# Performance work log

Hardware: AMD Instinct MI355X
Metric: run time of the kernel (lower is better)

The kernel has to match this reference:

```python
import jax, jax.numpy as jnp
import numpy as np

NUM_PARTS = 2
SAMPLE_STEP = 3  # models sample_points(pts, 3, True) as deterministic stride-3 subsampling


def quat_to_rot(q):
    # wxyz quaternion -> 3x3 rotation (same formula as the torch module)
    q = q / jnp.linalg.norm(q)
    a, b, c, d = q[0], q[1], q[2], q[3]
    return jnp.stack([
        1 - 2 * c * c - 2 * d * d, 2 * b * c - 2 * a * d, 2 * a * c + 2 * b * d,
        2 * b * c + 2 * a * d, 1 - 2 * b * b - 2 * d * d, 2 * c * d - 2 * a * b,
        2 * b * d - 2 * a * c, 2 * a * b + 2 * c * d, 1 - 2 * b * b - 2 * c * c,
    ]).reshape(3, 3)


def make_transform(q, t):
    rot = quat_to_rot(q)                      # (3,3)
    top = jnp.concatenate([rot, t], axis=1)   # (3,4)
    bottom = jnp.array([[0.0, 0.0, 0.0, 1.0]], dtype=top.dtype)
    return jnp.concatenate([top, bottom], axis=0)  # (4,4)


def chamfer(x, y):
    # x: (M,4), y: (M,4) homogeneous points; symmetric chamfer of Euclidean cdist
    d2 = jnp.sum(x * x, -1)[:, None] + jnp.sum(y * y, -1)[None, :] - 2.0 * (x @ y.T)
    d = jnp.sqrt(jnp.maximum(d2, 0.0))
    return jnp.mean(jnp.min(d, axis=1)) + jnp.mean(jnp.min(d, axis=0))


def setup_inputs() -> dict:
    key = jax.random.key(0)
    ks = jax.random.split(key, 6)
    N = 24576
    camera_pts = jax.random.normal(ks[0], (NUM_PARTS, N, 3), dtype=jnp.float32)
    cad_pts = jax.random.normal(ks[1], (NUM_PARTS, N, 3), dtype=jnp.float32)
    part_weight = jax.random.uniform(ks[2], (NUM_PARTS + 1,), dtype=jnp.float32)
    rot_quat = jax.random.normal(ks[3], (NUM_PARTS, 4), dtype=jnp.float32)
    tra = jax.random.normal(ks[4], (NUM_PARTS, 3, 1), dtype=jnp.float32)
    joint_axes = jax.random.normal(ks[5], (NUM_PARTS, 2, 4), dtype=jnp.float32)
    return {"camera_pts": camera_pts, "cad_pts": cad_pts, "part_weight": part_weight,
            "rot_quat": rot_quat, "tra": tra, "joint_axes": joint_axes}


def reference(camera_pts, cad_pts, part_weight, rot_quat, tra, joint_axes):
    # stride-3 subsample, then homogenize with a ones column
    scad = cad_pts[:, ::SAMPLE_STEP]      # (P, M, 3)
    scam = camera_pts[:, ::SAMPLE_STEP]   # (P, M, 3)
    ones = jnp.ones(scad.shape[:-1] + (1,), dtype=scad.dtype)
    scad_h = jnp.concatenate([scad, ones], axis=-1)  # (P, M, 4)
    scam_h = jnp.concatenate([scam, ones], axis=-1)  # (P, M, 4)

    transforms = jax.vmap(make_transform)(rot_quat, tra)        # (P, 4, 4)
    cad_base = jnp.einsum('pij,pnj->pni', transforms, scad_h)   # (P, M, 4)

    e_geo_parts = jax.vmap(chamfer)(cad_base, scam_h)           # (P,)
    e_geo = jnp.dot(part_weight[:NUM_PARTS], e_geo_parts)

    diff = transforms[0] @ joint_axes[0].T - transforms[1] @ joint_axes[1].T  # (4, K)
    e_kin = jax.nn.sigmoid(-5.0 * jnp.linalg.norm(diff))

    all_objective = e_geo + part_weight[NUM_PARTS] * e_kin
    return all_objective, e_kin, jax.lax.stop_gradient(transforms)
```

## Files before the change

kernel.cpp:

```cpp
#include <hip/hip_runtime.h>
#include <math.h>

#define NS 8192
#define NPTS 24576

#define BXC 64
#define XPT 16
#define XB (NS / (BXC * XPT))
#define YSPLIT 64
#define YTILE (NS / YSPLIT)

#define RB 256
#define RBLOCKS (4 * (NS / RB))

typedef __attribute__((ext_vector_type(2))) float f32x2;


__device__ inline void build_transform(const float* __restrict__ rot_quat,
                                       const float* __restrict__ tra,
                                       int p, float* t) {
    float a = rot_quat[p * 4 + 0], b = rot_quat[p * 4 + 1];
    float c = rot_quat[p * 4 + 2], d = rot_quat[p * 4 + 3];
    float inv = rsqrtf(a * a + b * b + c * c + d * d);
    a *= inv; b *= inv; c *= inv; d *= inv;
    t[0]  = 1.f - 2.f * c * c - 2.f * d * d;
    t[1]  = 2.f * b * c - 2.f * a * d;
    t[2]  = 2.f * a * c + 2.f * b * d;
    t[3]  = tra[p * 3 + 0];
    t[4]  = 2.f * b * c + 2.f * a * d;
    t[5]  = 1.f - 2.f * b * b - 2.f * d * d;
    t[6]  = 2.f * c * d - 2.f * a * b;
    t[7]  = tra[p * 3 + 1];
    t[8]  = 2.f * b * d - 2.f * a * c;
    t[9]  = 2.f * a * b + 2.f * c * d;
    t[10] = 1.f - 2.f * b * b - 2.f * c * c;
    t[11] = tra[p * 3 + 2];
    t[12] = 0.f; t[13] = 0.f; t[14] = 0.f; t[15] = 1.f;
}

__global__ void pack_kernel(const float* __restrict__ cam_pts,
                            const float* __restrict__ cad_pts,
                            const float* __restrict__ rot_quat,
                            const float* __restrict__ tra,
                            const float* __restrict__ joint_axes,
                            float* __restrict__ ws,
                            float4* __restrict__ pts,
                            float* __restrict__ out) {
    int gid = blockIdx.x * blockDim.x + threadIdx.x;
    int p = gid >> 13;
    int i = gid & (NS - 1);

    float T[16];
    build_transform(rot_quat, tra, p, T);

    int base = p * NPTS * 3 + i * 9;
    float x = cad_pts[base], y = cad_pts[base + 1], z = cad_pts[base + 2];
    float q0 = fmaf(T[0], x, fmaf(T[1], y, fmaf(T[2],  z, T[3])));
    float q1 = fmaf(T[4], x, fmaf(T[5], y, fmaf(T[6],  z, T[7])));
    float q2 = fmaf(T[8], x, fmaf(T[9], y, fmaf(T[10], z, T[11])));
    pts[p * NS + i] = make_float4(q0, q1, q2, fmaf(q0, q0, fmaf(q1, q1, q2 * q2)));
    float cx = cam_pts[base], cy = cam_pts[base + 1], cz = cam_pts[base + 2];
    pts[2 * NS + p * NS + i] =
        make_float4(cx, cy, cz, fmaf(cx, cx, fmaf(cy, cy, cz * cz)));

    if (gid == 0) {
        float T0[16], T1[16];
        build_transform(rot_quat, tra, 0, T0);
        build_transform(rot_quat, tra, 1, T1);
        for (int k = 0; k < 16; ++k) { out[2 + k] = T0[k]; out[18 + k] = T1[k]; }
        float ss = 0.f;
        for (int r = 0; r < 4; ++r)
            for (int j = 0; j < 2; ++j) {
                float d0 = 0.f, d1 = 0.f;
                for (int k = 0; k < 4; ++k) {
                    d0 += T0[r * 4 + k] * joint_axes[j * 4 + k];
                    d1 += T1[r * 4 + k] * joint_axes[8 + j * 4 + k];
                }
                float df = d0 - d1;
                ss += df * df;
            }
        float ek = 1.f / (1.f + expf(5.f * sqrtf(ss)));
        ws[36] = ek;
        out[1] = ek;
        ws[0] = 0.f; ws[1] = 0.f; ws[2] = 0.f; ws[3] = 0.f;
        ((unsigned*)ws)[37] = 0u;
    }
}

__global__ __launch_bounds__(BXC) void chamfer_kernel(const float4* __restrict__ pts,
                                                      float* __restrict__ partial) {
    int combo = blockIdx.y;
    int p   = combo >> 1;
    int dir = combo & 1;
    const float4* X = pts + (dir == 0 ? p * NS : 2 * NS + p * NS);
    const float4* Y = pts + (dir == 0 ? 2 * NS + p * NS : p * NS);
    int ys = blockIdx.z;
    int xb = blockIdx.x;
    int t  = threadIdx.x;

    __shared__ float4 sy[YTILE];

    int xbase = xb * (BXC * XPT) + t;
    f32x2 m0[XPT / 2], m1[XPT / 2], m2[XPT / 2], s[XPT / 2], dmin[XPT / 2];
#pragma unroll
    for (int g = 0; g < XPT / 2; ++g) {
        float4 v0 = X[xbase + (2 * g) * BXC];
        float4 v1 = X[xbase + (2 * g + 1) * BXC];
        m0[g] = (f32x2){-2.f * v0.x, -2.f * v1.x};
        m1[g] = (f32x2){-2.f * v0.y, -2.f * v1.y};
        m2[g] = (f32x2){-2.f * v0.z, -2.f * v1.z};
        s[g]  = (f32x2){v0.w, v1.w};
        dmin[g] = (f32x2){3.4e38f, 3.4e38f};
    }

    int ybase = ys * YTILE;
#pragma unroll
    for (int c = 0; c < YTILE / BXC; ++c)
        sy[t + c * BXC] = Y[ybase + c * BXC + t];
    __syncthreads();

#pragma unroll 4
    for (int j = 0; j < YTILE; ++j) {
        float4 y = sy[j];
        f32x2 yw = (f32x2){y.w, y.w};
        f32x2 yx = (f32x2){y.x, y.x};
        f32x2 yy = (f32x2){y.y, y.y};
        f32x2 yz = (f32x2){y.z, y.z};
#pragma unroll
        for (int g = 0; g < XPT / 2; ++g) {
            f32x2 d = __builtin_elementwise_fma(m0[g], yx, yw);
            d = __builtin_elementwise_fma(m1[g], yy, d);
            d = __builtin_elementwise_fma(m2[g], yz, d);
            dmin[g] = __builtin_elementwise_min(dmin[g], d);
        }
    }

    float* prow = partial + (combo * YSPLIT + ys) * NS + xbase;
#pragma unroll
    for (int g = 0; g < XPT / 2; ++g) {
        f32x2 v = dmin[g] + s[g];
        prow[(2 * g) * BXC]     = v.x;
        prow[(2 * g + 1) * BXC] = v.y;
    }
}

__global__ void reduce_kernel(const float* __restrict__ partial,
                              const float* __restrict__ pw,
                              float* __restrict__ ws,
                              float* __restrict__ out) {
    int combo = blockIdx.y;
    int x = blockIdx.x * RB + threadIdx.x;
    const float* p = partial + combo * (YSPLIT * NS) + x;
    float m = 3.4e38f;
#pragma unroll 8
    for (int ysi = 0; ysi < YSPLIT; ++ysi) m = fminf(m, p[ysi * NS]);
    float d = sqrtf(fmaxf(m, 0.f));
#pragma unroll
    for (int off = 32; off > 0; off >>= 1) d += __shfl_down(d, off, 64);
    __shared__ float sm[RB / 64];
    int wid = threadIdx.x >> 6;
    if ((threadIdx.x & 63) == 0) sm[wid] = d;
    __syncthreads();
    if (threadIdx.x == 0) {
        float sum = 0.f;
        for (int w = 0; w < RB / 64; ++w) sum += sm[w];
        atomicAdd(&ws[combo], sum);
        __threadfence();
        unsigned old = atomicAdd(&((unsigned*)ws)[37], 1u);
        if (old == RBLOCKS - 1) {
            float a0 = atomicAdd(&ws[0], 0.f);
            float a1 = atomicAdd(&ws[1], 0.f);
            float a2 = atomicAdd(&ws[2], 0.f);
            float a3 = atomicAdd(&ws[3], 0.f);
            float e0 = (a0 + a1) * (1.f / NS);
            float e1 = (a2 + a3) * (1.f / NS);
            out[0] = pw[0] * e0 + pw[1] * e1 + pw[2] * ws[36];
        }
    }
}

extern "C" void kernel_launch(void* const* d_in, const int* in_sizes, int n_in,
                              void* d_out, int out_size, void* d_ws, size_t ws_size,
                              hipStream_t stream) {
    const float* cam = (const float*)d_in[0];
    const float* cad = (const float*)d_in[1];
    const float* pw  = (const float*)d_in[2];
    const float* rq  = (const float*)d_in[3];
    const float* tr  = (const float*)d_in[4];
    const float* ja  = (const float*)d_in[5];
    float* out = (float*)d_out;
    float* ws  = (float*)d_ws;
    float4* pts = (float4*)(ws + 64);
    float* partial = ws + 64 + 16 * NS;

    pack_kernel<<<(2 * NS) / 256, 256, 0, stream>>>(cam, cad, rq, tr, ja, ws, pts, out);
    dim3 cg(XB, 4, YSPLIT);
    chamfer_kernel<<<cg, BXC, 0, stream>>>(pts, partial);
    reduce_kernel<<<dim3(NS / RB, 4), RB, 0, stream>>>(partial, pw, ws, out);
}
```

Measured before the change: 105.2 us.

## Fuse point packing and transform into chamfer kernel, drop pack launch

Removes the separate pack kernel. Each chamfer block now loads the raw strided points itself, applies the rigid transform and computes squared norms on the fly. The transform output, the kinematic term and the workspace zeroing move into one designated thread of the chamfer kernel. This saves a kernel launch and the intermediate float4 buffer round-trip, but it repeats the transform and the strided (stride-9 float) global loads in every block, about 8 blocks per y tile.

```diff
diff --git a/kernel.cpp b/kernel.cpp
--- a/kernel.cpp
+++ b/kernel.cpp
@@ -16,9 +16,9 @@
 typedef __attribute__((ext_vector_type(2))) float f32x2;
 
 
-__device__ inline void build_transform(const float* __restrict__ rot_quat,
-                                       const float* __restrict__ tra,
-                                       int p, float* t) {
+__device__ inline void build_transform12(const float* __restrict__ rot_quat,
+                                         const float* __restrict__ tra,
+                                         int p, float* t) {
     float a = rot_quat[p * 4 + 0], b = rot_quat[p * 4 + 1];
     float c = rot_quat[p * 4 + 2], d = rot_quat[p * 4 + 3];
     float inv = rsqrtf(a * a + b * b + c * c + d * d);
@@ -35,46 +35,119 @@
     t[9]  = 2.f * a * b + 2.f * c * d;
     t[10] = 1.f - 2.f * b * b - 2.f * c * c;
     t[11] = tra[p * 3 + 2];
-    t[12] = 0.f; t[13] = 0.f; t[14] = 0.f; t[15] = 1.f;
-}
-
-__global__ void pack_kernel(const float* __restrict__ cam_pts,
-                            const float* __restrict__ cad_pts,
-                            const float* __restrict__ rot_quat,
-                            const float* __restrict__ tra,
-                            const float* __restrict__ joint_axes,
-                            float* __restrict__ ws,
-                            float4* __restrict__ pts,
-                            float* __restrict__ out) {
-    int gid = blockIdx.x * blockDim.x + threadIdx.x;
-    int p = gid >> 13;
-    int i = gid & (NS - 1);
-
-    float T[16];
-    build_transform(rot_quat, tra, p, T);
-
-    int base = p * NPTS * 3 + i * 9;
-    float x = cad_pts[base], y = cad_pts[base + 1], z = cad_pts[base + 2];
-    float q0 = fmaf(T[0], x, fmaf(T[1], y, fmaf(T[2],  z, T[3])));
-    float q1 = fmaf(T[4], x, fmaf(T[5], y, fmaf(T[6],  z, T[7])));
-    float q2 = fmaf(T[8], x, fmaf(T[9], y, fmaf(T[10], z, T[11])));
-    pts[p * NS + i] = make_float4(q0, q1, q2, fmaf(q0, q0, fmaf(q1, q1, q2 * q2)));
-    float cx = cam_pts[base], cy = cam_pts[base + 1], cz = cam_pts[base + 2];
-    pts[2 * NS + p * NS + i] =
-        make_float4(cx, cy, cz, fmaf(cx, cx, fmaf(cy, cy, cz * cz)));
-
-    if (gid == 0) {
-        float T0[16], T1[16];
-        build_transform(rot_quat, tra, 0, T0);
-        build_transform(rot_quat, tra, 1, T1);
-        for (int k = 0; k < 16; ++k) { out[2 + k] = T0[k]; out[18 + k] = T1[k]; }
+}
+
+__global__ __launch_bounds__(BXC) void chamfer_kernel(
+        const float* __restrict__ cam_pts,
+        const float* __restrict__ cad_pts,
+        const float* __restrict__ rot_quat,
+        const float* __restrict__ tra,
+        const float* __restrict__ joint_axes,
+        float* __restrict__ ws,
+        float* __restrict__ partial,
+        float* __restrict__ out) {
+    int combo = blockIdx.y;
+    int p   = combo >> 1;
+    int dir = combo & 1;
+    int ys = blockIdx.z;
+    int xb = blockIdx.x;
+    int t  = threadIdx.x;
+
+    float T[12];
+    build_transform12(rot_quat, tra, p, T);
+
+    const float* xsrc = (dir == 0) ? cad_pts : cam_pts;
+    const float* ysrc = (dir == 0) ? cam_pts : cad_pts;
+    const int pbase = p * NPTS * 3;
+
+    __shared__ float4 sy[YTILE];
+
+    int ybase = ys * YTILE;
+#pragma unroll
+    for (int c = 0; c < YTILE / BXC; ++c) {
+        int idx = ybase + c * BXC + t;
+        int g = pbase + idx * 9;
+        float x = ysrc[g], y = ysrc[g + 1], z = ysrc[g + 2];
+        float q0, q1, q2;
+        if (dir == 1) {
+            q0 = fmaf(T[0], x, fmaf(T[1], y, fmaf(T[2],  z, T[3])));
+            q1 = fmaf(T[4], x, fmaf(T[5], y, fmaf(T[6],  z, T[7])));
+            q2 = fmaf(T[8], x, fmaf(T[9], y, fmaf(T[10], z, T[11])));
+        } else {
+            q0 = x; q1 = y; q2 = z;
+        }
+        sy[c * BXC + t] =
+            make_float4(q0, q1, q2, fmaf(q0, q0, fmaf(q1, q1, q2 * q2)));
+    }
+
+    int xbase = xb * (BXC * XPT) + t;
+    f32x2 m0[XPT / 2], m1[XPT / 2], m2[XPT / 2], s[XPT / 2], dmin[XPT / 2];
+#pragma unroll
+    for (int g = 0; g < XPT / 2; ++g) {
+        float q[2][3];
+#pragma unroll
+        for (int h = 0; h < 2; ++h) {
+            int idx = xbase + (2 * g + h) * BXC;
+            int gb = pbase + idx * 9;
+            float x = xsrc[gb], y = xsrc[gb + 1], z = xsrc[gb + 2];
+            if (dir == 0) {
+                q[h][0] = fmaf(T[0], x, fmaf(T[1], y, fmaf(T[2],  z, T[3])));
+                q[h][1] = fmaf(T[4], x, fmaf(T[5], y, fmaf(T[6],  z, T[7])));
+                q[h][2] = fmaf(T[8], x, fmaf(T[9], y, fmaf(T[10], z, T[11])));
+            } else {
+                q[h][0] = x; q[h][1] = y; q[h][2] = z;
+            }
+        }
+        m0[g] = (f32x2){-2.f * q[0][0], -2.f * q[1][0]};
+        m1[g] = (f32x2){-2.f * q[0][1], -2.f * q[1][1]};
+        m2[g] = (f32x2){-2.f * q[0][2], -2.f * q[1][2]};
+        s[g]  = (f32x2){
+            fmaf(q[0][0], q[0][0], fmaf(q[0][1], q[0][1], q[0][2] * q[0][2])),
+            fmaf(q[1][0], q[1][0], fmaf(q[1][1], q[1][1], q[1][2] * q[1][2]))};
+        dmin[g] = (f32x2){3.4e38f, 3.4e38f};
+    }
+    __syncthreads();
+
+#pragma unroll 4
+    for (int j = 0; j < YTILE; ++j) {
+        float4 y = sy[j];
+        f32x2 yw = (f32x2){y.w, y.w};
+        f32x2 yx = (f32x2){y.x, y.x};
+        f32x2 yy = (f32x2){y.y, y.y};
+        f32x2 yz = (f32x2){y.z, y.z};
+#pragma unroll
+        for (int g = 0; g < XPT / 2; ++g) {
+            f32x2 d = __builtin_elementwise_fma(m0[g], yx, yw);
+            d = __builtin_elementwise_fma(m1[g], yy, d);
+            d = __builtin_elementwise_fma(m2[g], yz, d);
+            dmin[g] = __builtin_elementwise_min(dmin[g], d);
+        }
+    }
+
+    float* prow = partial + (combo * YSPLIT + ys) * NS + xbase;
+#pragma unroll
+    for (int g = 0; g < XPT / 2; ++g) {
+        f32x2 v = dmin[g] + s[g];
+        prow[(2 * g) * BXC]     = v.x;
+        prow[(2 * g + 1) * BXC] = v.y;
+    }
+
+    if (xb == 0 && combo == 0 && ys == 0 && t == 0) {
+        float T0[12], T1[12];
+        build_transform12(rot_quat, tra, 0, T0);
+        build_transform12(rot_quat, tra, 1, T1);
+        for (int k = 0; k < 12; ++k) { out[2 + k] = T0[k]; out[18 + k] = T1[k]; }
+        out[14] = 0.f; out[15] = 0.f; out[16] = 0.f; out[17] = 1.f;
+        out[30] = 0.f; out[31] = 0.f; out[32] = 0.f; out[33] = 1.f;
         float ss = 0.f;
         for (int r = 0; r < 4; ++r)
             for (int j = 0; j < 2; ++j) {
                 float d0 = 0.f, d1 = 0.f;
                 for (int k = 0; k < 4; ++k) {
-                    d0 += T0[r * 4 + k] * joint_axes[j * 4 + k];
-                    d1 += T1[r * 4 + k] * joint_axes[8 + j * 4 + k];
+                    float t0k = (r < 3) ? T0[r * 4 + k] : ((k == 3) ? 1.f : 0.f);
+                    float t1k = (r < 3) ? T1[r * 4 + k] : ((k == 3) ? 1.f : 0.f);
+                    d0 += t0k * joint_axes[j * 4 + k];
+                    d1 += t1k * joint_axes[8 + j * 4 + k];
                 }
                 float df = d0 - d1;
                 ss += df * df;
@@ -84,63 +157,6 @@
         out[1] = ek;
         ws[0] = 0.f; ws[1] = 0.f; ws[2] = 0.f; ws[3] = 0.f;
         ((unsigned*)ws)[37] = 0u;
-    }
-}
-
-__global__ __launch_bounds__(BXC) void chamfer_kernel(const float4* __restrict__ pts,
-                                                      float* __restrict__ partial) {
-    int combo = blockIdx.y;
-    int p   = combo >> 1;
-    int dir = combo & 1;
-    const float4* X = pts + (dir == 0 ? p * NS : 2 * NS + p * NS);
-    const float4* Y = pts + (dir == 0 ? 2 * NS + p * NS : p * NS);
-    int ys = blockIdx.z;
-    int xb = blockIdx.x;
-    int t  = threadIdx.x;
-
-    __shared__ float4 sy[YTILE];
-
-    int xbase = xb * (BXC * XPT) + t;
-    f32x2 m0[XPT / 2], m1[XPT / 2], m2[XPT / 2], s[XPT / 2], dmin[XPT / 2];
-#pragma unroll
-    for (int g = 0; g < XPT / 2; ++g) {
-        float4 v0 = X[xbase + (2 * g) * BXC];
-        float4 v1 = X[xbase + (2 * g + 1) * BXC];
-        m0[g] = (f32x2){-2.f * v0.x, -2.f * v1.x};
-        m1[g] = (f32x2){-2.f * v0.y, -2.f * v1.y};
-        m2[g] = (f32x2){-2.f * v0.z, -2.f * v1.z};
-        s[g]  = (f32x2){v0.w, v1.w};
-        dmin[g] = (f32x2){3.4e38f, 3.4e38f};
-    }
-
-    int ybase = ys * YTILE;
-#pragma unroll
-    for (int c = 0; c < YTILE / BXC; ++c)
-        sy[t + c * BXC] = Y[ybase + c * BXC + t];
-    __syncthreads();
-
-#pragma unroll 4
-    for (int j = 0; j < YTILE; ++j) {
-        float4 y = sy[j];
-        f32x2 yw = (f32x2){y.w, y.w};
-        f32x2 yx = (f32x2){y.x, y.x};
-        f32x2 yy = (f32x2){y.y, y.y};
-        f32x2 yz = (f32x2){y.z, y.z};
-#pragma unroll
-        for (int g = 0; g < XPT / 2; ++g) {
-            f32x2 d = __builtin_elementwise_fma(m0[g], yx, yw);
-            d = __builtin_elementwise_fma(m1[g], yy, d);
-            d = __builtin_elementwise_fma(m2[g], yz, d);
-            dmin[g] = __builtin_elementwise_min(dmin[g], d);
-        }
-    }
-
-    float* prow = partial + (combo * YSPLIT + ys) * NS + xbase;
-#pragma unroll
-    for (int g = 0; g < XPT / 2; ++g) {
-        f32x2 v = dmin[g] + s[g];
-        prow[(2 * g) * BXC]     = v.x;
-        prow[(2 * g + 1) * BXC] = v.y;
     }
 }
 
@@ -190,11 +206,9 @@
     const float* ja  = (const float*)d_in[5];
     float* out = (float*)d_out;
     float* ws  = (float*)d_ws;
-    float4* pts = (float4*)(ws + 64);
-    float* partial = ws + 64 + 16 * NS;
-
-    pack_kernel<<<(2 * NS) / 256, 256, 0, stream>>>(cam, cad, rq, tr, ja, ws, pts, out);
+    float* partial = ws + 64;
+
     dim3 cg(XB, 4, YSPLIT);
-    chamfer_kernel<<<cg, BXC, 0, stream>>>(pts, partial);
+    chamfer_kernel<<<cg, BXC, 0, stream>>>(cam, cad, rq, tr, ja, ws, partial, out);
     reduce_kernel<<<dim3(NS / RB, 4), RB, 0, stream>>>(partial, pw, ws, out);
 }
```

Result: no change. 105.3 us (+0.1%).
